# Optimization experiments

Measured on AMD Instinct MI355X. Metric: run time of the kernel, lower is better.

## Reference

```python
import jax, jax.numpy as jnp
import numpy as np
from jax import lax

EPS = 1e-5
K = 3  # DCN kernel size


def _conv(x, w, pad, lhs_dil=(1, 1)):
    return lax.conv_general_dilated(
        x, w, window_strides=(1, 1), padding=((pad, pad), (pad, pad)),
        lhs_dilation=lhs_dil, dimension_numbers=('NCHW', 'OIHW', 'NCHW'))


def _batchnorm(x, gamma, beta):
    # training-mode BN (batch statistics), matching nn.BatchNorm2d in train()
    m = jnp.mean(x, axis=(0, 2, 3), keepdims=True)
    v = jnp.var(x, axis=(0, 2, 3), keepdims=True)
    return (x - m) * lax.rsqrt(v + EPS) * gamma[None, :, None, None] + beta[None, :, None, None]


def _bilinear_sample(x, py, px):
    # x: [B,C,H,W]; py,px: [B,K2,H,W] fractional sample coords (zero-pad outside)
    B, C, H, W = x.shape
    K2 = py.shape[1]
    y0 = jnp.floor(py)
    x0 = jnp.floor(px)
    wy = (py - y0)[:, None]  # [B,1,K2,H,W]
    wx = (px - x0)[:, None]
    xf = x.reshape(B, C, H * W)

    def gather(yi, xi):
        valid = ((yi >= 0) & (yi <= H - 1) & (xi >= 0) & (xi <= W - 1)).astype(x.dtype)
        yc = jnp.clip(yi, 0, H - 1).astype(jnp.int32)
        xc = jnp.clip(xi, 0, W - 1).astype(jnp.int32)
        idx = (yc * W + xc).reshape(B, 1, -1)
        v = jnp.take_along_axis(xf, idx, axis=2).reshape(B, C, K2, H, W)
        return v * valid[:, None]

    v00 = gather(y0, x0)
    v01 = gather(y0, x0 + 1)
    v10 = gather(y0 + 1, x0)
    v11 = gather(y0 + 1, x0 + 1)
    return (v00 * (1 - wy) * (1 - wx) + v01 * (1 - wy) * wx
            + v10 * wy * (1 - wx) + v11 * wy * wx)  # [B,C,K2,H,W]


def _dcn(x, w_off, b_off, w_dcn, b_dcn):
    # Modulated deformable conv (DCNv2), stride 1, pad 1, dil 1, 1 deform group
    B, C, H, W = x.shape
    K2 = K * K
    om = _conv(x, w_off, pad=1) + b_off[None, :, None, None]  # [B,3*K2,H,W]
    dy, dx, m = om[:, :K2], om[:, K2:2 * K2], jax.nn.sigmoid(om[:, 2 * K2:])
    ki, kj = jnp.meshgrid(jnp.arange(K), jnp.arange(K), indexing='ij')
    ky = (ki.reshape(-1) - 1).astype(x.dtype)[None, :, None, None]
    kx = (kj.reshape(-1) - 1).astype(x.dtype)[None, :, None, None]
    py = dy + jnp.arange(H, dtype=x.dtype)[None, None, :, None] + ky
    px = dx + jnp.arange(W, dtype=x.dtype)[None, None, None, :] + kx
    val = _bilinear_sample(x, py, px) * m[:, None]  # [B,C,K2,H,W]
    Co = w_dcn.shape[0]
    out = jnp.einsum('bikhw,oik->bohw', val, w_dcn.reshape(Co, C, K2))
    return out + b_dcn[None, :, None, None]


def _conv_transpose(x, w_up):
    # torch ConvTranspose2d(k=4, stride=2, pad=1), weight [Cin, Cout, 4, 4]
    w = jnp.flip(w_up, axis=(2, 3)).transpose(1, 0, 2, 3)  # -> OIHW
    return _conv(x, w, pad=2, lhs_dil=(2, 2))


def setup_inputs() -> dict:
    key = jax.random.key(0)
    ks = jax.random.split(key, 8)
    B, Cin, Cout, H, W = 4, 256, 256, 64, 64
    x = jax.random.normal(ks[0], (B, Cin, H, W), dtype=jnp.float32)
    w_off = jax.random.normal(ks[1], (3 * K * K, Cin, K, K), dtype=jnp.float32) * 0.01
    b_off = jnp.zeros((3 * K * K,), dtype=jnp.float32)
    w_dcn = jax.random.normal(ks[2], (Cout, Cin, K, K), dtype=jnp.float32) * (1.0 / np.sqrt(Cin * K * K))
    b_dcn = jnp.zeros((Cout,), dtype=jnp.float32)
    gamma1 = jax.random.uniform(ks[3], (Cout,), dtype=jnp.float32, minval=0.5, maxval=1.5)
    beta1 = jax.random.normal(ks[4], (Cout,), dtype=jnp.float32) * 0.1
    w_up = jax.random.normal(ks[5], (Cout, Cout, 4, 4), dtype=jnp.float32) * (1.0 / np.sqrt(Cout * 16))
    gamma2 = jax.random.uniform(ks[6], (Cout,), dtype=jnp.float32, minval=0.5, maxval=1.5)
    beta2 = jax.random.normal(ks[7], (Cout,), dtype=jnp.float32) * 0.1
    return {'x': x, 'w_off': w_off, 'b_off': b_off, 'w_dcn': w_dcn, 'b_dcn': b_dcn,
            'gamma1': gamma1, 'beta1': beta1, 'w_up': w_up, 'gamma2': gamma2, 'beta2': beta2}


def reference(x, w_off, b_off, w_dcn, b_dcn, gamma1, beta1, w_up, gamma2, beta2):
    out = _dcn(x, w_off, b_off, w_dcn, b_dcn)
    out = jax.nn.relu(_batchnorm(out, gamma1, beta1))
    out = _conv_transpose(out, w_up)
    out = jax.nn.relu(_batchnorm(out, gamma2, beta2))
    return out
```

## Files before the change

kernel.cpp:

```cpp
#include <hip/hip_runtime.h>
#include <hip/hip_bf16.h>
#include <math.h>

#define B_   4
#define CIN  256
#define COUT 256
#define HW   4096

typedef __attribute__((ext_vector_type(8))) short short8;
typedef __attribute__((ext_vector_type(4))) float float4v;

#define LSTR  40
#define LSTR2 72
#define LSTR4 136

__device__ __forceinline__ float sigmoidf_(float v){ return 1.0f/(1.0f+expf(-v)); }
__device__ __forceinline__ ushort f2bf(float f){
  union { float f; unsigned u; } x; x.f = f;
  unsigned r = x.u + 0x7fffu + ((x.u>>16)&1u);
  return (ushort)(r>>16);
}
__device__ __forceinline__ float bflo(unsigned u){ union{unsigned u; float f;} c; c.u = u<<16;          return c.f; }
__device__ __forceinline__ float bfhi(unsigned u){ union{unsigned u; float f;} c; c.u = u & 0xffff0000u; return c.f; }

__global__ void k_transpose_x(const float* __restrict__ x, ushort* __restrict__ xtb){
  __shared__ float ts[32][33];
  int tx = threadIdx.x & 31, ty = threadIdx.x >> 5;
  int p0 = blockIdx.x * 32, c0 = blockIdx.y * 32, b = blockIdx.z;
  const float* xb = x + (size_t)b*CIN*HW;
#pragma unroll
  for(int q=0;q<4;q++){
    int c = ty + q*8;
    ts[c][tx] = xb[(size_t)(c0+c)*HW + p0+tx];
  }
  __syncthreads();
#pragma unroll
  for(int q=0;q<4;q++){
    int pr = ty + q*8;
    xtb[((size_t)(b*HW + p0+pr)<<8) + c0+tx] = f2bf(ts[tx][pr]);
  }
}

__global__ void k_build_Wob(const float* __restrict__ w_off, ushort* __restrict__ Wob){
  int f = blockIdx.x*256 + threadIdx.x;
  int kc = f>>10, o = (f>>5)&31, kk = f&31;
  int k = kc*32 + kk, tap = k>>8, c = k&255;
  float v = (o < 27) ? w_off[(size_t)o*2304 + c*9 + tap] : 0.f;
  Wob[f] = f2bf(v);
}
__global__ void k_build_Wdb(const float* __restrict__ w_dcn, ushort* __restrict__ Wdb){
  int f = blockIdx.x*256 + threadIdx.x;
  int kc = f>>13, o = (f>>5)&255, kk = f&31;
  int k = kc>>3, c = ((kc&7)<<5) | kk;
  Wdb[f] = f2bf(w_dcn[(size_t)o*2304 + c*9 + k]);
}
__global__ void k_build_WT2c(const float* __restrict__ w_up, ushort* __restrict__ WT2c){
  int f = blockIdx.x*256 + threadIdx.x;
  int pp = f>>18, kc = (f>>13)&31, o = (f>>5)&255, kk = f&31;
  int k = kc*32 + kk, ab = k>>8, c = k&255;
  int a = ab>>1, bb = ab&1, ph = pp>>1, pw = pp&1;
  WT2c[f] = f2bf(w_up[(size_t)(c*COUT+o)*16 + (3-ph-2*a)*4 + (3-pw-2*bb)]);
}

__global__ __launch_bounds__(256) void k_offset_mfma(const ushort* __restrict__ xtb,
                        const ushort* __restrict__ Wob, float* __restrict__ om){
  __shared__ ushort Vs[2][64*LSTR4];
  __shared__ int sIdx[576];
  int tid = threadIdx.x;
  int px0 = blockIdx.x * 64;
  int b   = blockIdx.y;
  for(int t=tid; t<576; t+=256){
    int tap = t>>6, px = t&63;
    int p = px0+px, hh = p>>6, ww = p&63;
    int ih = hh + tap/3 - 1, iw = ww + tap%3 - 1;
    sIdx[t] = (ih>=0 && ih<64 && iw>=0 && iw<64) ? ((b*HW + ih*64+iw)<<8) : -1;
  }
  __syncthreads();

  int lane = tid&63, wv = tid>>6, lo = lane&15, hi = lane>>4;
  float4v acc[2];
  acc[0] = acc[1] = (float4v){0.f,0.f,0.f,0.f};
  int vpx = tid>>2, vseg = tid&3;
  const int wlane = lo*32 + hi*8;

#define OFF_WLOAD_ALLQ(Q, W) do{ \
    _Pragma("unroll") \
    for(int c_=0;c_<4;c_++){ \
      const ushort* wp_ = Wob + (((Q)*4+c_)<<10) + wlane; \
      W[2*c_+0] = *(const short8*)(wp_); \
      W[2*c_+1] = *(const short8*)(wp_ + 512); \
    } \
  }while(0)

#define OFF_GATHER_Q(Q, V) do{ \
    int k_ = (Q)>>1, c0_ = ((Q)&1)<<7; \
    int idx_ = sIdx[(k_<<6)+vpx]; \
    int coff_ = c0_ + (vseg<<5); \
    V[0]=make_uint4(0,0,0,0); V[1]=make_uint4(0,0,0,0); \
    V[2]=make_uint4(0,0,0,0); V[3]=make_uint4(0,0,0,0); \
    if(idx_ >= 0){ \
      V[0] = *(const uint4*)(xtb + idx_ + coff_); \
      V[1] = *(const uint4*)(xtb + idx_ + coff_ + 8); \
      V[2] = *(const uint4*)(xtb + idx_ + coff_ + 16); \
      V[3] = *(const uint4*)(xtb + idx_ + coff_ + 24); \
    } \
  }while(0)

#define OFF_VWRITE_Q(V, BUF) do{ \
    ushort* vp_ = &Vs[BUF][vpx*LSTR4 + (vseg<<5)]; \
    *(uint4*)(vp_)      = V[0]; \
    *(uint4*)(vp_ + 8)  = V[1]; \
    *(uint4*)(vp_ + 16) = V[2]; \
    *(uint4*)(vp_ + 24) = V[3]; \
  }while(0)

#define OFF_COMPUTE_Q2(W, BUF) do{ \
    const ushort* bp_ = &Vs[BUF][(wv*16+lo)*LSTR4 + hi*8]; \
    _Pragma("unroll") \
    for(int c_=0;c_<4;c_++){ \
      short8 ba_ = *(const short8*)(bp_ + c_*32); \
      acc[0] = __builtin_amdgcn_mfma_f32_16x16x32_bf16(W[2*c_+0], ba_, acc[0], 0,0,0); \
      acc[1] = __builtin_amdgcn_mfma_f32_16x16x32_bf16(W[2*c_+1], ba_, acc[1], 0,0,0); \
    } \
  }while(0)

  short8 w[8];
  uint4 vE[4], vO[4];
  OFF_GATHER_Q(0, vE);
  OFF_VWRITE_Q(vE, 0);
  OFF_GATHER_Q(1, vO);
  __syncthreads();

#pragma unroll 1
  for(int pb=0; pb<18; pb+=2){
    {
      OFF_WLOAD_ALLQ(pb, w);
      if(pb<16) OFF_GATHER_Q(pb+2, vE);
      OFF_COMPUTE_Q2(w, 0);
      OFF_VWRITE_Q(vO, 1);
      __syncthreads();
    }
    {
      OFF_WLOAD_ALLQ(pb+1, w);
      if(pb<15) OFF_GATHER_Q(pb+3, vO);
      OFF_COMPUTE_Q2(w, 1);
      if(pb<16) OFF_VWRITE_Q(vE, 0);
      __syncthreads();
    }
  }
  int p = px0 + wv*16 + lo;
#pragma unroll
  for(int mi=0;mi<2;mi++){
    int ob = mi*16 + hi*4;
    float4v a = (mi==0) ? acc[0] : acc[1];
#pragma unroll
    for(int r=0;r<4;r++){
      int o = ob + r;
      if(o < 27) om[(size_t)(b*27+o)*HW + p] = a[r];
    }
  }
}

#define DCN_WLOAD_ALLQ(Q, W) do{ \
    _Pragma("unroll") \
    for(int c_=0;c_<4;c_++){ \
      const ushort* wp_ = Wdb + ((size_t)((Q)*4+c_)<<13) + wlane; \
      W[4*c_+0] = *(const short8*)(wp_); \
      W[4*c_+1] = *(const short8*)(wp_ + 512); \
      W[4*c_+2] = *(const short8*)(wp_ + 1024); \
      W[4*c_+3] = *(const short8*)(wp_ + 1536); \
    } \
  }while(0)

#define DCN_GATHER_Q(Q, C, CF) do{ \
    int k_ = (Q)>>1, c0_ = ((Q)&1)<<7; \
    int t_ = (k_<<6) + vpx; \
    int pk_ = sPk[t_]; CF = sCf[t_]; \
    int coff_ = c0_ + (vseg<<4); \
    int iy0_=pk_&63, iy1_=(pk_>>6)&63, ix0_=(pk_>>12)&63, ix1_=(pk_>>18)&63; \
    const ushort* p00_ = xtb + cbase + (((iy0_<<6)+ix0_)<<8) + coff_; \
    const ushort* p01_ = xtb + cbase + (((iy0_<<6)+ix1_)<<8) + coff_; \
    const ushort* p10_ = xtb + cbase + (((iy1_<<6)+ix0_)<<8) + coff_; \
    const ushort* p11_ = xtb + cbase + (((iy1_<<6)+ix1_)<<8) + coff_; \
    C[0] = *(const uint4*)(p00_);     C[4] = *(const uint4*)(p00_ + 8); \
    C[1] = *(const uint4*)(p01_);     C[5] = *(const uint4*)(p01_ + 8); \
    C[2] = *(const uint4*)(p10_);     C[6] = *(const uint4*)(p10_ + 8); \
    C[3] = *(const uint4*)(p11_);     C[7] = *(const uint4*)(p11_ + 8); \
  }while(0)

#define DCN_BLEND_H(C0,C1,C2,C3, CF, DST) do{ \
    union{ ushort us[8]; uint4 q; } rr_; \
    rr_.us[0] = f2bf(CF.x*bflo(C0.x)+CF.y*bflo(C1.x)+CF.z*bflo(C2.x)+CF.w*bflo(C3.x)); \
    rr_.us[1] = f2bf(CF.x*bfhi(C0.x)+CF.y*bfhi(C1.x)+CF.z*bfhi(C2.x)+CF.w*bfhi(C3.x)); \
    rr_.us[2] = f2bf(CF.x*bflo(C0.y)+CF.y*bflo(C1.y)+CF.z*bflo(C2.y)+CF.w*bflo(C3.y)); \
    rr_.us[3] = f2bf(CF.x*bfhi(C0.y)+CF.y*bfhi(C1.y)+CF.z*bfhi(C2.y)+CF.w*bfhi(C3.y)); \
    rr_.us[4] = f2bf(CF.x*bflo(C0.z)+CF.y*bflo(C1.z)+CF.z*bflo(C2.z)+CF.w*bflo(C3.z)); \
    rr_.us[5] = f2bf(CF.x*bfhi(C0.z)+CF.y*bfhi(C1.z)+CF.z*bfhi(C2.z)+CF.w*bfhi(C3.z)); \
    rr_.us[6] = f2bf(CF.x*bflo(C0.w)+CF.y*bflo(C1.w)+CF.z*bflo(C2.w)+CF.w*bflo(C3.w)); \
    rr_.us[7] = f2bf(CF.x*bfhi(C0.w)+CF.y*bfhi(C1.w)+CF.z*bfhi(C2.w)+CF.w*bfhi(C3.w)); \
    *(uint4*)(DST) = rr_.q; \
  }while(0)

#define DCN_BLEND_Q(C, CF, BUF) do{ \
    ushort* dp_ = &Vs[BUF][vpx*LSTR4 + (vseg<<4)]; \
    DCN_BLEND_H(C[0],C[1],C[2],C[3], CF, dp_); \
    DCN_BLEND_H(C[4],C[5],C[6],C[7], CF, dp_ + 8); \
  }while(0)

#define DCN_COMPUTE_Q2(W, BUF) do{ \
    const ushort* bp_ = &Vs[BUF][(pn0+lo)*LSTR4 + hi*8]; \
    _Pragma("unroll") \
    for(int c_=0;c_<4;c_++){ \
      short8 b0_ = *(const short8*)(bp_ + c_*32); \
      short8 b1_ = *(const short8*)(bp_ + c_*32 + 16*LSTR4); \
      acc[0][0] = __builtin_amdgcn_mfma_f32_16x16x32_bf16(W[4*c_+0], b0_, acc[0][0], 0,0,0); \
      acc[0][1] = __builtin_amdgcn_mfma_f32_16x16x32_bf16(W[4*c_+0], b1_, acc[0][1], 0,0,0); \
      acc[1][0] = __builtin_amdgcn_mfma_f32_16x16x32_bf16(W[4*c_+1], b0_, acc[1][0], 0,0,0); \
      acc[1][1] = __builtin_amdgcn_mfma_f32_16x16x32_bf16(W[4*c_+1], b1_, acc[1][1], 0,0,0); \
      acc[2][0] = __builtin_amdgcn_mfma_f32_16x16x32_bf16(W[4*c_+2], b0_, acc[2][0], 0,0,0); \
      acc[2][1] = __builtin_amdgcn_mfma_f32_16x16x32_bf16(W[4*c_+2], b1_, acc[2][1], 0,0,0); \
      acc[3][0] = __builtin_amdgcn_mfma_f32_16x16x32_bf16(W[4*c_+3], b0_, acc[3][0], 0,0,0); \
      acc[3][1] = __builtin_amdgcn_mfma_f32_16x16x32_bf16(W[4*c_+3], b1_, acc[3][1], 0,0,0); \
    } \
  }while(0)

__global__ __launch_bounds__(512) void k_dcn_mfma(const ushort* __restrict__ xtb,
                        const float* __restrict__ om, const float* __restrict__ b_off,
                        const ushort* __restrict__ Wdb, float* __restrict__ out1){
  __shared__ ushort Vs[2][64*LSTR4];
  __shared__ int    sPk[576];
  __shared__ float4 sCf[576];
  int tid = threadIdx.x;
  int px0 = blockIdx.x * 64;
  int b   = blockIdx.y;

  for(int t=tid; t<576; t+=512){
    int k = t>>6, px = t&63;
    int p = px0 + px, hh = p>>6, ww = p&63;
    const float* omp = om + (size_t)b*27*HW + p;
    float dy = omp[(size_t)k*HW]      + b_off[k];
    float dx = omp[(size_t)(9+k)*HW]  + b_off[9+k];
    float mo = sigmoidf_(omp[(size_t)(18+k)*HW] + b_off[18+k]);
    float py  = dy + (float)(hh + k/3 - 1);
    float pxf = dx + (float)(ww + k%3 - 1);
    float y0 = floorf(py), x0 = floorf(pxf);
    float wy = py - y0, wx = pxf - x0;
    float y1 = y0 + 1.0f, x1 = x0 + 1.0f;
    bool vy0 = (y0>=0.f)&&(y0<=63.f), vy1 = (y1>=0.f)&&(y1<=63.f);
    bool vx0 = (x0>=0.f)&&(x0<=63.f), vx1 = (x1>=0.f)&&(x1<=63.f);
    int iy0 = (int)fminf(fmaxf(y0,0.f),63.f);
    int iy1 = (int)fminf(fmaxf(y1,0.f),63.f);
    int ix0 = (int)fminf(fmaxf(x0,0.f),63.f);
    int ix1 = (int)fminf(fmaxf(x1,0.f),63.f);
    sPk[t] = iy0 | (iy1<<6) | (ix0<<12) | (ix1<<18);
    sCf[t] = make_float4((vy0&&vx0)? (1.f-wy)*(1.f-wx)*mo : 0.f,
                         (vy0&&vx1)? (1.f-wy)*wx*mo       : 0.f,
                         (vy1&&vx0)? wy*(1.f-wx)*mo       : 0.f,
                         (vy1&&vx1)? wy*wx*mo             : 0.f);
  }
  __syncthreads();

  int lane = tid&63, wv = tid>>6, lo = lane&15, hi = lane>>4;
  int om0 = (wv>>1)*64, pn0 = (wv&1)*32;
  float4v acc[4][2];
#pragma unroll
  for(int i=0;i<4;i++)
#pragma unroll
    for(int j=0;j<2;j++) acc[i][j] = (float4v){0.f,0.f,0.f,0.f};
  int cbase = (b*HW)<<8;
  int vpx = tid>>3, vseg = tid&7;
  const int wlane = (om0+lo)*32 + hi*8;

  short8 w[16];
  uint4 cE[8], cO[8];
  float4 fE, fO;

  DCN_GATHER_Q(0, cE, fE);
  DCN_BLEND_Q(cE, fE, 0);
  DCN_GATHER_Q(1, cO, fO);
  __syncthreads();

#pragma unroll 1
  for(int pb=0; pb<18; pb+=2){
    {
      DCN_WLOAD_ALLQ(pb, w);
      if(pb<16) DCN_GATHER_Q(pb+2, cE, fE);
      DCN_COMPUTE_Q2(w, 0);
      DCN_BLEND_Q(cO, fO, 1);
      __syncthreads();
    }
    {
      DCN_WLOAD_ALLQ(pb+1, w);
      if(pb<15) DCN_GATHER_Q(pb+3, cO, fO);
      DCN_COMPUTE_Q2(w, 1);
      if(pb<16) DCN_BLEND_Q(cE, fE, 0);
      __syncthreads();
    }
  }

#pragma unroll
  for(int i=0;i<4;i++){
    int ob = om0 + i*16 + hi*4;
#pragma unroll
    for(int r=0;r<4;r++){
      int o = ob + r;
      float* op = out1 + (size_t)(b*COUT + o)*HW + px0 + pn0 + lo;
#pragma unroll
      for(int j=0;j<2;j++) op[j*16] = acc[i][j][r];
    }
  }
}

__global__ void k_bn_stats(const float* __restrict__ xin, float* __restrict__ stats, int per_b){
  int o = blockIdx.x, tid = threadIdx.x;
  float s=0.f, ss=0.f;
  for(int b=0;b<B_;b++){
    const float* p = xin + (size_t)(b*COUT+o)*per_b;
    for(int i=tid;i<per_b;i+=256){ float v = p[i]; s+=v; ss+=v*v; }
  }
  __shared__ float rs[256], rss[256];
  rs[tid]=s; rss[tid]=ss; __syncthreads();
  for(int st=128; st>0; st>>=1){
    if(tid<st){ rs[tid]+=rs[tid+st]; rss[tid]+=rss[tid+st]; }
    __syncthreads();
  }
  if(tid==0){
    float n = (float)(B_*per_b);
    float mean = rs[0]/n;
    float var  = rss[0]/n - mean*mean;
    stats[o*2] = mean; stats[o*2+1] = rsqrtf(var + 1e-5f);
  }
}

__global__ void k_bn_stats_ct(const ushort* __restrict__ ct, float* __restrict__ stats){
  int o = blockIdx.x, tid = threadIdx.x;
  float s=0.f, ss=0.f;
  for(int pl=0; pl<16; ++pl){
    const ushort* p = ct + (((size_t)(pl*256 + o))<<12);
    for(int i=tid*8; i<4096; i+=2048){
      uint4 v = *(const uint4*)(p + i);
      float f;
      f=bflo(v.x); s+=f; ss+=f*f;  f=bfhi(v.x); s+=f; ss+=f*f;
      f=bflo(v.y); s+=f; ss+=f*f;  f=bfhi(v.y); s+=f; ss+=f*f;
      f=bflo(v.z); s+=f; ss+=f*f;  f=bfhi(v.z); s+=f; ss+=f*f;
      f=bflo(v.w); s+=f; ss+=f*f;  f=bfhi(v.w); s+=f; ss+=f*f;
    }
  }
  __shared__ float rs[256], rss[256];
  rs[tid]=s; rss[tid]=ss; __syncthreads();
  for(int st=128; st>0; st>>=1){
    if(tid<st){ rs[tid]+=rs[tid+st]; rss[tid]+=rss[tid+st]; }
    __syncthreads();
  }
  if(tid==0){
    float n = (float)(16*4096);
    float mean = rs[0]/n;
    float var  = rss[0]/n - mean*mean;
    stats[o*2] = mean; stats[o*2+1] = rsqrtf(var + 1e-5f);
  }
}

__global__ void k_bn1_apply_t(const float* __restrict__ out1, const float* __restrict__ stats,
                              const float* __restrict__ gamma, const float* __restrict__ beta,
                              ushort* __restrict__ y1b){
  __shared__ float ts[32][33];
  int tx = threadIdx.x & 31, ty = threadIdx.x >> 5;
  int p0 = blockIdx.x*32, o0 = blockIdx.y*32, b = blockIdx.z;
#pragma unroll
  for(int q=0;q<4;q++){
    int oo = ty + q*8; int o = o0 + oo;
    float m = stats[o*2], rstd = stats[o*2+1];
    float scale = rstd * gamma[o];
    float shift = beta[o] - m * scale;
    float v = out1[(size_t)(b*COUT+o)*HW + p0+tx];
    ts[oo][tx] = fmaxf(v*scale + shift, 0.f);
  }
  __syncthreads();
#pragma unroll
  for(int q=0;q<4;q++){
    int pr = ty + q*8;
    y1b[((size_t)(b*HW + p0+pr)<<8) + o0+tx] = f2bf(ts[tx][pr]);
  }
}

__global__ __launch_bounds__(512) void k_convt_mfma(const ushort* __restrict__ y1b,
                        const ushort* __restrict__ WT2c,
                        ushort* __restrict__ ct){
  __shared__ ushort Vs[2][256*LSTR2];
  __shared__ int sIdx[1024];
  int tid = threadIdx.x;
  int px0 = blockIdx.x * 256;
  int b   = blockIdx.y;
  int pp  = blockIdx.z;
  int ph = pp>>1, pw = pp&1;

  for(int t=tid; t<1024; t+=512){
    int ab = t>>8, px = t&255;
    int a = ab>>1, bb = ab&1;
    int p = px0+px, r = p>>6, s = p&63;
    int ih = r + ph - 1 + a, iw = s + pw - 1 + bb;
    sIdx[t] = (ih>=0 && ih<64 && iw>=0 && iw<64) ? ((b*HW + ih*64+iw)<<8) : -1;
  }
  __syncthreads();

  int lane = tid&63, wv = tid>>6, lo = lane&15, hi = lane>>4;
  int om0 = (wv>>1)*64;
  int pn0 = (wv&1)*128;
  float4v acc[4][8];
#pragma unroll
  for(int i=0;i<4;i++)
#pragma unroll
    for(int j=0;j<8;j++) acc[i][j] = (float4v){0.f,0.f,0.f,0.f};

  const ushort* wbase = WT2c + ((size_t)pp<<18);
  const int wlaneb = (om0+lo)*32 + hi*8;
  int vpx = tid>>1, vseg = tid&1;
  uint4 vpre[4];

#define CT3_PREFETCH(PC) do{ \
    int kc0_ = (PC)*2; \
    int ab_ = kc0_>>3, c0_ = (kc0_&7)<<5; \
    int idx_ = sIdx[(ab_<<8) + vpx]; \
    int co_ = c0_ + vseg*32; \
    vpre[0]=make_uint4(0,0,0,0); vpre[1]=make_uint4(0,0,0,0); \
    vpre[2]=make_uint4(0,0,0,0); vpre[3]=make_uint4(0,0,0,0); \
    if(idx_ >= 0){ \
      vpre[0] = *(const uint4*)(y1b + idx_ + co_); \
      vpre[1] = *(const uint4*)(y1b + idx_ + co_ + 8); \
      vpre[2] = *(const uint4*)(y1b + idx_ + co_ + 16); \
      vpre[3] = *(const uint4*)(y1b + idx_ + co_ + 24); \
    } \
  }while(0)

#define CT3_WRITE(BUF) do{ \
    ushort* vp_ = &Vs[BUF][vpx*LSTR2 + vseg*32]; \
    *(uint4*)(vp_)      = vpre[0]; \
    *(uint4*)(vp_ + 8)  = vpre[1]; \
    *(uint4*)(vp_ + 16) = vpre[2]; \
    *(uint4*)(vp_ + 24) = vpre[3]; \
  }while(0)

  CT3_PREFETCH(0);
  CT3_WRITE(0);
  __syncthreads();

#pragma unroll 1
  for(int pc=0; pc<16; ++pc){
    int cur = pc&1;
    if(pc < 15) CT3_PREFETCH(pc+1);
#pragma unroll
    for(int c=0; c<2; ++c){
      const ushort* wp = wbase + ((size_t)(((pc<<1)|c))<<13) + wlaneb;
      const ushort* bp = &Vs[cur][(pn0+lo)*LSTR2 + c*32 + hi*8];
      short8 bfr[8];
#pragma unroll
      for(int j=0;j<8;j++) bfr[j] = *(const short8*)(bp + j*16*LSTR2);
#pragma unroll
      for(int i=0;i<4;i++){
        short8 afr = *(const short8*)(wp + i*512);
#pragma unroll
        for(int j=0;j<8;j++)
          acc[i][j] = __builtin_amdgcn_mfma_f32_16x16x32_bf16(afr, bfr[j], acc[i][j], 0,0,0);
      }
    }
    if(pc < 15) CT3_WRITE(cur^1);
    __syncthreads();
  }

  ushort* cb = ct + (((size_t)(pp*4 + b)*256)<<12);
#pragma unroll
  for(int i=0;i<4;i++){
#pragma unroll
    for(int r=0;r<4;r++){
      int o = om0 + i*16 + hi*4 + r;
      ushort* row = cb + ((size_t)o<<12) + px0 + pn0 + lo;
#pragma unroll
      for(int j=0;j<8;j++) row[j*16] = f2bf(acc[i][j][r]);
    }
  }
}

__global__ void k_bn2_apply(const ushort* __restrict__ ct, const float* __restrict__ stats,
                            const float* __restrict__ gamma, const float* __restrict__ beta,
                            float* __restrict__ out){
  int gid = blockIdx.x*256 + threadIdx.x;
  int e4 = gid<<2;
  int b = e4>>22, o = (e4>>14)&255, q = e4&16383;
  int H2 = q>>7, W2 = q&127;
  int r = H2>>1, ph = H2&1, s0 = W2>>1;
  size_t base0 = (((size_t)((ph*2)*4 + b)*256 + o)<<12) + r*64 + s0;
  unsigned u0 = *(const unsigned*)(ct + base0);
  unsigned u1 = *(const unsigned*)(ct + base0 + ((size_t)4<<20));
  float m = stats[o*2], rstd = stats[o*2+1];
  float sc = rstd * gamma[o];
  float sh = beta[o] - m * sc;
  float4 v;
  v.x = fmaxf(bflo(u0)*sc + sh, 0.f);
  v.y = fmaxf(bflo(u1)*sc + sh, 0.f);
  v.z = fmaxf(bfhi(u0)*sc + sh, 0.f);
  v.w = fmaxf(bfhi(u1)*sc + sh, 0.f);
  *(float4*)(out + e4) = v;
}

extern "C" void kernel_launch(void* const* d_in, const int* in_sizes, int n_in,
                              void* d_out, int out_size, void* d_ws, size_t ws_size,
                              hipStream_t stream){
  (void)in_sizes; (void)n_in; (void)out_size; (void)ws_size;
  const float* x     = (const float*)d_in[0];
  const float* w_off = (const float*)d_in[1];
  const float* b_off = (const float*)d_in[2];
  const float* w_dcn = (const float*)d_in[3];
  const float* gamma1= (const float*)d_in[5];
  const float* beta1 = (const float*)d_in[6];
  const float* w_up  = (const float*)d_in[7];
  const float* gamma2= (const float*)d_in[8];
  const float* beta2 = (const float*)d_in[9];
  float* out = (float*)d_out;

  float* ws   = (float*)d_ws;
  ushort* ct  = (ushort*)ws;
  float* om   = ws;
  ushort* xtb = (ushort*)(ws + 442368);
  float* out1 = ws + 442368 + 2097152;
  float* base2 = ws + 8388608;
  ushort* y1b  = (ushort*)base2;
  ushort* WT2c = (ushort*)(base2 + 2097152);
  ushort* Wdb  = (ushort*)(base2 + 2097152 + 524288);
  ushort* Wob  = (ushort*)(base2 + 2097152 + 524288 + 294912);
  float* st1   = base2 + 2097152 + 524288 + 294912 + 36864;
  float* st2   = st1 + 512;

  k_transpose_x <<<dim3(128,8,4), 256, 0, stream>>>(x, xtb);
  k_build_Wob   <<<288,  256, 0, stream>>>(w_off, Wob);
  k_build_Wdb   <<<2304, 256, 0, stream>>>(w_dcn, Wdb);
  k_build_WT2c  <<<4096, 256, 0, stream>>>(w_up, WT2c);
  k_offset_mfma <<<dim3(64,4),  256, 0, stream>>>(xtb, Wob, om);
  k_dcn_mfma    <<<dim3(64,4),  512, 0, stream>>>(xtb, om, b_off, Wdb, out1);
  k_bn_stats    <<<256,  256, 0, stream>>>(out1, st1, 4096);
  k_bn1_apply_t <<<dim3(128,8,4), 256, 0, stream>>>(out1, st1, gamma1, beta1, y1b);
  k_convt_mfma  <<<dim3(16,4,4),  512, 0, stream>>>(y1b, WT2c, ct);
  k_bn_stats_ct <<<256,  256, 0, stream>>>(ct, st2);
  k_bn2_apply   <<<16384,256, 0, stream>>>(ct, st2, gamma2, beta2, out);
}
```

Measured before the change: 274.8 us.

## Merge weight-prep kernels and remap block indices for XCD-aware scheduling

Merges the three weight-repacking kernels into one launch that branches on block index, removing two kernel launches and the gaps between them. It also remaps the flat block id in the offset, DCN and transposed-conv kernels so that neighbouring blocks, which are likely spread across different XCDs, get different batch/pixel tiles. The intent is better L2 locality per XCD for the shared input and weight data. The remapping assumes the grid dimensions stay exactly as written.

New measurement: 267.8 us. 1.03x faster.

```diff
diff --git a/kernel.cpp b/kernel.cpp
--- a/kernel.cpp
+++ b/kernel.cpp
@@ -41,25 +41,29 @@
   }
 }
 
-__global__ void k_build_Wob(const float* __restrict__ w_off, ushort* __restrict__ Wob){
-  int f = blockIdx.x*256 + threadIdx.x;
-  int kc = f>>10, o = (f>>5)&31, kk = f&31;
-  int k = kc*32 + kk, tap = k>>8, c = k&255;
-  float v = (o < 27) ? w_off[(size_t)o*2304 + c*9 + tap] : 0.f;
-  Wob[f] = f2bf(v);
-}
-__global__ void k_build_Wdb(const float* __restrict__ w_dcn, ushort* __restrict__ Wdb){
-  int f = blockIdx.x*256 + threadIdx.x;
-  int kc = f>>13, o = (f>>5)&255, kk = f&31;
-  int k = kc>>3, c = ((kc&7)<<5) | kk;
-  Wdb[f] = f2bf(w_dcn[(size_t)o*2304 + c*9 + k]);
-}
-__global__ void k_build_WT2c(const float* __restrict__ w_up, ushort* __restrict__ WT2c){
-  int f = blockIdx.x*256 + threadIdx.x;
-  int pp = f>>18, kc = (f>>13)&31, o = (f>>5)&255, kk = f&31;
-  int k = kc*32 + kk, ab = k>>8, c = k&255;
-  int a = ab>>1, bb = ab&1, ph = pp>>1, pw = pp&1;
-  WT2c[f] = f2bf(w_up[(size_t)(c*COUT+o)*16 + (3-ph-2*a)*4 + (3-pw-2*bb)]);
+__global__ void k_build_all(const float* __restrict__ w_off, const float* __restrict__ w_dcn,
+                            const float* __restrict__ w_up,
+                            ushort* __restrict__ Wob, ushort* __restrict__ Wdb,
+                            ushort* __restrict__ WT2c){
+  int bid = blockIdx.x;
+  if(bid < 288){
+    int f = bid*256 + threadIdx.x;
+    int kc = f>>10, o = (f>>5)&31, kk = f&31;
+    int k = kc*32 + kk, tap = k>>8, c = k&255;
+    float v = (o < 27) ? w_off[(size_t)o*2304 + c*9 + tap] : 0.f;
+    Wob[f] = f2bf(v);
+  } else if(bid < 288+2304){
+    int f = (bid-288)*256 + threadIdx.x;
+    int kc = f>>13, o = (f>>5)&255, kk = f&31;
+    int k = kc>>3, c = ((kc&7)<<5) | kk;
+    Wdb[f] = f2bf(w_dcn[(size_t)o*2304 + c*9 + k]);
+  } else {
+    int f = (bid-2592)*256 + threadIdx.x;
+    int pp = f>>18, kc = (f>>13)&31, o = (f>>5)&255, kk = f&31;
+    int k = kc*32 + kk, ab = k>>8, c = k&255;
+    int a = ab>>1, bb = ab&1, ph = pp>>1, pw = pp&1;
+    WT2c[f] = f2bf(w_up[(size_t)(c*COUT+o)*16 + (3-ph-2*a)*4 + (3-pw-2*bb)]);
+  }
 }
 
 __global__ __launch_bounds__(256) void k_offset_mfma(const ushort* __restrict__ xtb,
@@ -67,8 +71,9 @@
   __shared__ ushort Vs[2][64*LSTR4];
   __shared__ int sIdx[576];
   int tid = threadIdx.x;
-  int px0 = blockIdx.x * 64;
-  int b   = blockIdx.y;
+  int fb  = blockIdx.x + (blockIdx.y<<6);
+  int b   = (fb&7)>>1;
+  int px0 = ((((fb>>3)<<1) | (fb&1))) << 6;
   for(int t=tid; t<576; t+=256){
     int tap = t>>6, px = t&63;
     int p = px0+px, hh = p>>6, ww = p&63;
@@ -231,8 +236,9 @@
   __shared__ int    sPk[576];
   __shared__ float4 sCf[576];
   int tid = threadIdx.x;
-  int px0 = blockIdx.x * 64;
-  int b   = blockIdx.y;
+  int fb  = blockIdx.x + (blockIdx.y<<6);
+  int b   = (fb&7)>>1;
+  int px0 = ((((fb>>3)<<1) | (fb&1))) << 6;
 
   for(int t=tid; t<576; t+=512){
     int k = t>>6, px = t&63;
@@ -389,9 +395,11 @@
   __shared__ ushort Vs[2][256*LSTR2];
   __shared__ int sIdx[1024];
   int tid = threadIdx.x;
-  int px0 = blockIdx.x * 256;
-  int b   = blockIdx.y;
-  int pp  = blockIdx.z;
+  int fb  = blockIdx.x + (blockIdx.y<<4) + (blockIdx.z<<6);
+  int jj = fb&7, rr2 = fb>>3;
+  int b   = jj>>1;
+  int pp  = ((rr2>>4)<<1) | (jj&1);
+  int px0 = (rr2&15) << 8;
   int ph = pp>>1, pw = pp&1;
 
   for(int t=tid; t<1024; t+=512){
@@ -531,9 +539,7 @@
   float* st2   = st1 + 512;
 
   k_transpose_x <<<dim3(128,8,4), 256, 0, stream>>>(x, xtb);
-  k_build_Wob   <<<288,  256, 0, stream>>>(w_off, Wob);
-  k_build_Wdb   <<<2304, 256, 0, stream>>>(w_dcn, Wdb);
-  k_build_WT2c  <<<4096, 256, 0, stream>>>(w_up, WT2c);
+  k_build_all   <<<6688, 256, 0, stream>>>(w_off, w_dcn, w_up, Wob, Wdb, WT2c);
   k_offset_mfma <<<dim3(64,4),  256, 0, stream>>>(xtb, Wob, om);
   k_dcn_mfma    <<<dim3(64,4),  512, 0, stream>>>(xtb, om, b_off, Wdb, out1);
   k_bn_stats    <<<256,  256, 0, stream>>>(out1, st1, 4096);
```
